# Kernel optimization log

Hardware: AMD Instinct MI355X
Metric: run time of the kernel (lower is better)

The kernel has to match this reference:

```python
import jax, jax.numpy as jnp
import numpy as np
from jax import lax

N = 1024          # proposals per image
C = 81            # classes incl. background
F = 1024          # feature dim
K = 100           # detections_per_img
IMG_W, IMG_H = 1216.0, 800.0
SCORE_THRESH = 0.05
NMS_THRESH = 0.5
BBOX_CLIP = float(np.log(1000.0 / 16.0))
WX, WY, WW, WH = 10.0, 10.0, 5.0, 5.0     # BoxCoder default weights


def setup_inputs() -> dict:
    key = jax.random.key(0)
    k1, k2, k3, k4, k5 = jax.random.split(key, 5)
    class_logits = jax.random.normal(k1, (N, C), jnp.float32) * 2.0
    box_regression = jax.random.normal(k2, (N, C * 4), jnp.float32) * 0.2
    xy = jax.random.uniform(k3, (N, 2), jnp.float32) * jnp.array([IMG_W * 0.7, IMG_H * 0.7], jnp.float32)
    wh = 16.0 + jax.random.uniform(k4, (N, 2), jnp.float32) * jnp.array([IMG_W * 0.3, IMG_H * 0.3], jnp.float32)
    proposal_boxes = jnp.concatenate([xy, xy + wh], axis=1)  # valid xyxy
    features = jax.random.normal(k5, (N, F), jnp.float32)
    return {"class_logits": class_logits, "box_regression": box_regression,
            "proposal_boxes": proposal_boxes, "features": features}


def _decode(rel, boxes):
    # BoxCoder.decode with weights (10,10,5,5), TO_REMOVE=1. rel:[N,C*4] boxes:[N,4] -> [N,C,4]
    rel = rel.reshape(N, C, 4)
    widths = boxes[:, 2] - boxes[:, 0] + 1.0
    heights = boxes[:, 3] - boxes[:, 1] + 1.0
    ctr_x = boxes[:, 0] + 0.5 * widths
    ctr_y = boxes[:, 1] + 0.5 * heights
    dx = rel[..., 0] / WX
    dy = rel[..., 1] / WY
    dw = jnp.minimum(rel[..., 2] / WW, BBOX_CLIP)
    dh = jnp.minimum(rel[..., 3] / WH, BBOX_CLIP)
    pcx = dx * widths[:, None] + ctr_x[:, None]
    pcy = dy * heights[:, None] + ctr_y[:, None]
    pw = jnp.exp(dw) * widths[:, None]
    ph = jnp.exp(dh) * heights[:, None]
    return jnp.stack([pcx - 0.5 * pw, pcy - 0.5 * ph,
                      pcx + 0.5 * pw - 1.0, pcy + 0.5 * ph - 1.0], axis=-1)


def _clip(b):
    # clip_to_image with TO_REMOVE=1
    x1 = jnp.clip(b[..., 0], 0.0, IMG_W - 1.0)
    y1 = jnp.clip(b[..., 1], 0.0, IMG_H - 1.0)
    x2 = jnp.clip(b[..., 2], 0.0, IMG_W - 1.0)
    y2 = jnp.clip(b[..., 3], 0.0, IMG_H - 1.0)
    return jnp.stack([x1, y1, x2, y2], axis=-1)


def _nms_class(boxes_c, scores_c, valid_c):
    # Sequential hard NMS for one class with fixed shapes. Invalid (below score
    # thresh) boxes can neither be kept nor suppress others.
    s_sort = jnp.where(valid_c, scores_c, -jnp.inf)
    order = jnp.argsort(-s_sort)              # descending score
    b = boxes_c[order]
    v = valid_c[order]
    s = scores_c[order]
    area = (b[:, 2] - b[:, 0] + 1.0) * (b[:, 3] - b[:, 1] + 1.0)
    lt = jnp.maximum(b[:, None, :2], b[None, :, :2])
    rb = jnp.minimum(b[:, None, 2:], b[None, :, 2:])
    whd = jnp.clip(rb - lt + 1.0, 0.0)
    inter = whd[..., 0] * whd[..., 1]
    iou = inter / (area[:, None] + area[None, :] - inter)  # [N,N]
    idx = jnp.arange(N)
    def body(i, keep):
        sup = (iou[i] > NMS_THRESH) & keep[i] & (idx > i)
        return keep & ~sup
    keep = lax.fori_loop(0, N, body, v)
    return b, order, jnp.where(keep, s, -1.0)


def reference(class_logits, box_regression, proposal_boxes, features):
    probs = jax.nn.softmax(class_logits, axis=-1)          # [N,C]
    dec = _clip(_decode(box_regression, proposal_boxes))    # [N,C,4]
    boxes_cls = jnp.transpose(dec[:, 1:, :], (1, 0, 2))     # [C-1,N,4] (skip background)
    scores_cls = probs[:, 1:].T                             # [C-1,N]
    valid = scores_cls > SCORE_THRESH
    b_s, order, s_kept = jax.vmap(_nms_class)(boxes_cls, scores_cls, valid)
    flat_s = s_kept.reshape(-1)                             # [(C-1)*N]
    top_s, top_i = lax.top_k(flat_s, K)
    cls_i = top_i // N
    pos_i = top_i % N
    boxes_out = b_s[cls_i, pos_i]                           # [K,4]
    orig = order[cls_i, pos_i]                              # original proposal idx
    feat_out = features[orig]                               # [K,F]
    labels = cls_i + 1
    ok = top_s > 0.0
    scores_out = jnp.where(ok, top_s, 0.0)
    boxes_out = jnp.where(ok[:, None], boxes_out, 0.0)
    feat_out = jnp.where(ok[:, None], feat_out, 0.0)
    labels = jnp.where(ok, labels, 0)
    return boxes_out, scores_out, feat_out, labels
```

## Files before the change

kernel.cpp:

```cpp
#include <hip/hip_runtime.h>
#include <math.h>

#define N 1024
#define C 81
#define F 1024
#define K 100
#define NC1 80
#define MAXC (NC1 * N)
#define HBASE 0x3D00
#define HSIZE 1024
#define SELCAP 2048

#define SCORE_THRESH 0.05f
#define NMS_THRESH   0.5f
#define BBOX_CLIP    4.135166556742356f
#define IMG_W1       1215.0f
#define IMG_H1       799.0f

typedef unsigned long long u64;
typedef unsigned int u32;

__global__ __launch_bounds__(256) void k_softmax_decode(
    const float* __restrict__ logits, const float* __restrict__ boxreg,
    const float* __restrict__ pboxes, float* __restrict__ probsT,
    float4* __restrict__ decT, int* __restrict__ hist, int* __restrict__ counter)
{
    int gid = blockIdx.x * 256 + threadIdx.x;
    if (gid < HSIZE) hist[gid] = 0;
    if (gid == 0) *counter = 0;

    int n = blockIdx.x * 4 + (threadIdx.x >> 6);
    int t = threadIdx.x & 63;

    float v1 = logits[n * C + t];
    float v2 = (t < C - 64) ? logits[n * C + 64 + t] : -INFINITY;
    float m = fmaxf(v1, v2);
    for (int off = 32; off; off >>= 1) m = fmaxf(m, __shfl_xor(m, off));
    float e1 = expf(v1 - m);
    float e2 = (t < C - 64) ? expf(v2 - m) : 0.0f;
    float s = e1 + e2;
    for (int off = 32; off; off >>= 1) s += __shfl_xor(s, off);

    probsT[t * N + n] = e1 / s;
    if (t < C - 64) probsT[(64 + t) * N + n] = e2 / s;

    float bx1 = pboxes[n * 4 + 0], by1 = pboxes[n * 4 + 1];
    float bx2 = pboxes[n * 4 + 2], by2 = pboxes[n * 4 + 3];
    float w  = bx2 - bx1 + 1.0f, h = by2 - by1 + 1.0f;
    float cx = bx1 + 0.5f * w,  cy = by1 + 0.5f * h;

    #pragma unroll
    for (int rep = 0; rep < 2; ++rep) {
        int cl = t + rep * 64;
        if (cl >= C) break;
        const float* r = boxreg + (size_t)n * (C * 4) + cl * 4;
        float dx = r[0] / 10.0f, dy = r[1] / 10.0f;
        float dw = fminf(r[2] / 5.0f, BBOX_CLIP);
        float dh = fminf(r[3] / 5.0f, BBOX_CLIP);

        float pcx = dx * w + cx, pcy = dy * h + cy;
        float pw = expf(dw) * w, ph = expf(dh) * h;

        float x1 = pcx - 0.5f * pw,        y1 = pcy - 0.5f * ph;
        float x2 = pcx + 0.5f * pw - 1.0f, y2 = pcy + 0.5f * ph - 1.0f;

        x1 = fminf(fmaxf(x1, 0.0f), IMG_W1);
        y1 = fminf(fmaxf(y1, 0.0f), IMG_H1);
        x2 = fminf(fmaxf(x2, 0.0f), IMG_W1);
        y2 = fminf(fmaxf(y2, 0.0f), IMG_H1);

        decT[(size_t)cl * N + n] = make_float4(x1, y1, x2, y2);
    }
}

__global__ __launch_bounds__(256) void k_nms(
    const float* __restrict__ probsT, const float4* __restrict__ decT,
    int* counter, u64* __restrict__ ckey, int* __restrict__ hist,
    int* __restrict__ corder)
{
    int c = blockIdx.x;
    int t = threadIdx.x;
    __shared__ u64    skey64[N];
    __shared__ int    scnt[256];
    __shared__ float4 sbox[N];
    __shared__ float  sarea[N];
    __shared__ int    skeep[N];

    const float4* prow = (const float4*)(probsT + (size_t)(c + 1) * N);
    float4 s4 = prow[t];
    int f0 = s4.x > SCORE_THRESH, f1 = s4.y > SCORE_THRESH;
    int f2 = s4.z > SCORE_THRESH, f3 = s4.w > SCORE_THRESH;
    int mycount = f0 + f1 + f2 + f3;
    scnt[t] = mycount;
    __syncthreads();
    for (int off = 1; off < 256; off <<= 1) {
        int v = scnt[t];
        int a = (t >= off) ? scnt[t - off] : 0;
        __syncthreads();
        scnt[t] = v + a;
        __syncthreads();
    }
    int base = scnt[t] - mycount;
    int V = scnt[255];
    {
        int p0 = t * 4, pos = base;
        if (f0) skey64[pos++] = ((u64)__float_as_uint(s4.x) << 32) | (u32)~(u32)(p0);
        if (f1) skey64[pos++] = ((u64)__float_as_uint(s4.y) << 32) | (u32)~(u32)(p0 + 1);
        if (f2) skey64[pos++] = ((u64)__float_as_uint(s4.z) << 32) | (u32)~(u32)(p0 + 2);
        if (f3) skey64[pos++] = ((u64)__float_as_uint(s4.w) << 32) | (u32)~(u32)(p0 + 3);
    }
    __syncthreads();
    if (V == 0) return;

    if (V <= 64) {
        if (t < 64) {
            int lane = t;
            u64 key = (lane < V) ? skey64[lane] : 0ull;
            for (int k = 2; k <= 64; k <<= 1) {
                for (int j = k >> 1; j > 0; j >>= 1) {
                    u64 other = __shfl_xor(key, j);
                    bool takeMax = (((lane & j) == 0) == ((lane & k) == 0));
                    bool gt = key > other;
                    key = (takeMax == gt) ? key : other;
                }
            }
            bool act = key != 0ull;
            float4 b = make_float4(0.f, 0.f, 0.f, 0.f);
            float area = 0.0f;
            if (act) {
                int idx = (int)(~(u32)(key & 0xffffffffu));
                corder[c * N + lane] = idx;
                b = decT[(size_t)(c + 1) * N + idx];
                area = (b.z - b.x + 1.0f) * (b.w - b.y + 1.0f);
            }
            int kept = act ? 1 : 0;
            for (int i = 0; i + 1 < V; ++i) {
                int   ki  = __shfl(kept, i);
                float bix = __shfl(b.x, i), biy = __shfl(b.y, i);
                float biz = __shfl(b.z, i), biw = __shfl(b.w, i);
                float ai  = __shfl(area, i);
                if (ki && lane > i && kept) {
                    float lx = fmaxf(bix, b.x), ly = fmaxf(biy, b.y);
                    float rx = fminf(biz, b.z), ry = fminf(biw, b.w);
                    float ww = fmaxf(rx - lx + 1.0f, 0.0f);
                    float hh = fmaxf(ry - ly + 1.0f, 0.0f);
                    float inter = ww * hh;
                    float iou = inter / (ai + area - inter);
                    if (iou > NMS_THRESH) kept = 0;
                }
            }
            if (kept) {
                int pos = atomicAdd(counter, 1);
                u32 sb = (u32)(key >> 32);
                ckey[pos] = ((u64)sb << 32) | (u64)(u32)~(u32)(c * N + lane);
                atomicAdd(&hist[(int)(sb >> 16) - HBASE], 1);
            }
        }
        return;
    }

    int P = 128;
    while (P < V) P <<= 1;
    for (int i = V + t; i < P; i += 256) skey64[i] = 0ull;
    __syncthreads();
    for (int k = 2; k <= P; k <<= 1) {
        for (int j = k >> 1; j > 0; j >>= 1) {
            for (int i = t; i < P; i += 256) {
                int ixj = i ^ j;
                if (ixj > i) {
                    u64 a = skey64[i], bb = skey64[ixj];
                    bool desc = ((i & k) == 0);
                    if (desc ? (a < bb) : (a > bb)) { skey64[i] = bb; skey64[ixj] = a; }
                }
            }
            __syncthreads();
        }
    }
    for (int p = t; p < V; p += 256) {
        int idx = (int)(~(u32)(skey64[p] & 0xffffffffu));
        corder[c * N + p] = idx;
        float4 b = decT[(size_t)(c + 1) * N + idx];
        sbox[p]  = b;
        sarea[p] = (b.z - b.x + 1.0f) * (b.w - b.y + 1.0f);
        skeep[p] = 1;
    }
    __syncthreads();
    for (int i = 0; i < V; ++i) {
        if (skeep[i]) {
            float4 bi = sbox[i];
            float  ai = sarea[i];
            for (int j = i + 1 + t; j < V; j += 256) {
                if (skeep[j]) {
                    float4 bj = sbox[j];
                    float lx = fmaxf(bi.x, bj.x), ly = fmaxf(bi.y, bj.y);
                    float rx = fminf(bi.z, bj.z), ry = fminf(bi.w, bj.w);
                    float ww = fmaxf(rx - lx + 1.0f, 0.0f);
                    float hh = fmaxf(ry - ly + 1.0f, 0.0f);
                    float inter = ww * hh;
                    float iou = inter / (ai + sarea[j] - inter);
                    if (iou > NMS_THRESH) skeep[j] = 0;
                }
            }
        }
        __syncthreads();
    }
    for (int p = t; p < V; p += 256) {
        if (skeep[p]) {
            int pos = atomicAdd(counter, 1);
            u32 sb = (u32)(skey64[p] >> 32);
            ckey[pos] = ((u64)sb << 32) | (u64)(u32)~(u32)(c * N + p);
            atomicAdd(&hist[(int)(sb >> 16) - HBASE], 1);
        }
    }
}

__global__ __launch_bounds__(1024) void k_select(
    const int* __restrict__ counter, u64* ckey, const int* __restrict__ hist,
    float* __restrict__ sel_score, int* __restrict__ sel_flat)
{
    int t = threadIdx.x;
    __shared__ u64 keys[SELCAP];
    __shared__ int partial[1024];
    __shared__ int sb_bstar, scount;
    __shared__ u64 wk[16];
    __shared__ int wp[16];

    int M = *counter;
    if (t == 0) { sb_bstar = 0; scount = 0; }

    int lsum = hist[t];
    partial[t] = lsum;
    __syncthreads();
    for (int off = 1; off < 1024; off <<= 1) {
        int v = partial[t];
        int a = (t + off < 1024) ? partial[t + off] : 0;
        __syncthreads();
        partial[t] = v + a;
        __syncthreads();
    }
    int base = partial[t] - lsum;
    if (base < K && base + lsum >= K) sb_bstar = t;
    __syncthreads();
    int bstar = sb_bstar;

    for (int p = t; p < M; p += 1024) {
        u64 kk = ckey[p];
        int b = (int)((kk >> 48) & 0xFFFF) - HBASE;
        if (b >= bstar) {
            int pos = atomicAdd(&scount, 1);
            if (pos < SELCAP) keys[pos] = kk;
        }
    }
    __syncthreads();
    int cnt = scount;

    if (cnt > SELCAP) {
        for (int k = 0; k < K; ++k) {
            u64 key = 0ull; int pos = -1;
            for (int p = t; p < M; p += 1024) {
                u64 kk = ckey[p];
                if (kk > key) { key = kk; pos = p; }
            }
            for (int off = 32; off; off >>= 1) {
                u64 ok2 = __shfl_down(key, off);
                int op = __shfl_down(pos, off);
                if (ok2 > key) { key = ok2; pos = op; }
            }
            if ((t & 63) == 0) { wk[t >> 6] = key; wp[t >> 6] = pos; }
            __syncthreads();
            if (t == 0) {
                for (int w = 1; w < 16; ++w)
                    if (wk[w] > key) { key = wk[w]; pos = wp[w]; }
                if (key != 0ull) {
                    sel_score[k] = __uint_as_float((u32)(key >> 32));
                    sel_flat[k]  = (int)(~(u32)(key & 0xffffffffu));
                    ckey[pos] = 0ull;
                } else { sel_score[k] = 0.0f; sel_flat[k] = 0; }
            }
            __syncthreads();
        }
        return;
    }

    int P = 128;
    while (P < cnt) P <<= 1;
    for (int i = cnt + t; i < P; i += 1024) keys[i] = 0ull;
    __syncthreads();
    for (int k = 2; k <= P; k <<= 1) {
        for (int j = k >> 1; j > 0; j >>= 1) {
            for (int i = t; i < P; i += 1024) {
                int ixj = i ^ j;
                if (ixj > i) {
                    u64 a = keys[i], b = keys[ixj];
                    bool desc = ((i & k) == 0);
                    if (desc ? (a < b) : (a > b)) { keys[i] = b; keys[ixj] = a; }
                }
            }
            __syncthreads();
        }
    }
    if (t < K) {
        u64 key = keys[t];
        sel_score[t] = __uint_as_float((u32)(key >> 32));
        sel_flat[t]  = (int)(~(u32)(key & 0xffffffffu));
    }
}

__global__ __launch_bounds__(256) void k_gather(
    const float* __restrict__ sel_score, const int* __restrict__ sel_flat,
    const int* __restrict__ corder, const float4* __restrict__ decT,
    const float* __restrict__ feats, float* __restrict__ out)
{
    int k = blockIdx.x, t = threadIdx.x;
    float s = sel_score[k];
    bool ok = s > 0.0f;
    float4 b = make_float4(0.f, 0.f, 0.f, 0.f);
    int label = 0, orig = 0;
    if (ok) {
        int flat = sel_flat[k];
        int c = flat >> 10;
        orig  = corder[flat];
        b     = decT[(size_t)(c + 1) * N + orig];
        label = c + 1;
    }
    if (t == 0) {
        out[k * 4 + 0] = b.x; out[k * 4 + 1] = b.y;
        out[k * 4 + 2] = b.z; out[k * 4 + 3] = b.w;
        out[K * 4 + k] = ok ? s : 0.0f;
        out[K * 4 + K + K * F + k] = (float)label;
    }
    const float4* src = (const float4*)(feats + (size_t)orig * F);
    float4* dst = (float4*)(out + K * 4 + K + (size_t)k * F);
    float4 z = make_float4(0.f, 0.f, 0.f, 0.f);
    if (t < F / 4) dst[t] = ok ? src[t] : z;
}

extern "C" void kernel_launch(void* const* d_in, const int* in_sizes, int n_in,
                              void* d_out, int out_size, void* d_ws, size_t ws_size,
                              hipStream_t stream)
{
    const float* logits = (const float*)d_in[0];
    const float* boxreg = (const float*)d_in[1];
    const float* pboxes = (const float*)d_in[2];
    const float* feats  = (const float*)d_in[3];
    float* out = (float*)d_out;

    char* ws = (char*)d_ws;
    size_t off = 0;
    auto alloc = [&](size_t bytes) {
        size_t cur = off;
        off = (off + bytes + 255) & ~(size_t)255;
        return cur;
    };
    int*    counter   = (int*)   (ws + alloc(sizeof(int)));
    float*  probsT    = (float*) (ws + alloc(sizeof(float)  * C * N));
    float4* decT      = (float4*)(ws + alloc(sizeof(float4) * C * N));
    u64*    ckey      = (u64*)   (ws + alloc(sizeof(u64)    * MAXC));
    int*    hist      = (int*)   (ws + alloc(sizeof(int)    * HSIZE));
    int*    corder    = (int*)   (ws + alloc(sizeof(int)    * NC1 * N));
    float*  sel_score = (float*) (ws + alloc(sizeof(float)  * K));
    int*    sel_flat  = (int*)   (ws + alloc(sizeof(int)    * K));

    hipLaunchKernelGGL(k_softmax_decode, dim3(N / 4), dim3(256), 0, stream,
                       logits, boxreg, pboxes, probsT, decT, hist, counter);
    hipLaunchKernelGGL(k_nms, dim3(NC1), dim3(256), 0, stream,
                       probsT, decT, counter, ckey, hist, corder);
    hipLaunchKernelGGL(k_select, dim3(1), dim3(1024), 0, stream,
                       counter, ckey, hist, sel_score, sel_flat);
    hipLaunchKernelGGL(k_gather, dim3(K), dim3(256), 0, stream,
                       sel_score, sel_flat, corder, decT, feats, out);
}
```

Baseline: 107.7 us.

## Fuse softmax and box decode into per-class NMS kernel, drop intermediate buffers

```diff
diff --git a/kernel.cpp b/kernel.cpp
--- a/kernel.cpp
+++ b/kernel.cpp
@@ -20,76 +20,75 @@
 typedef unsigned long long u64;
 typedef unsigned int u32;
 
-__global__ __launch_bounds__(256) void k_softmax_decode(
+__device__ float4 decode_box(const float* __restrict__ pboxes,
+                             const float* __restrict__ boxreg, int idx, int cl)
+{
+    float4 pb = ((const float4*)pboxes)[idx];
+    float4 r  = *(const float4*)(boxreg + (size_t)idx * (C * 4) + cl * 4);
+    float w  = pb.z - pb.x + 1.0f, h = pb.w - pb.y + 1.0f;
+    float cx = pb.x + 0.5f * w,  cy = pb.y + 0.5f * h;
+    float dx = r.x / 10.0f, dy = r.y / 10.0f;
+    float dw = fminf(r.z / 5.0f, BBOX_CLIP);
+    float dh = fminf(r.w / 5.0f, BBOX_CLIP);
+    float pcx = dx * w + cx, pcy = dy * h + cy;
+    float pw = expf(dw) * w, ph = expf(dh) * h;
+    float x1 = pcx - 0.5f * pw,        y1 = pcy - 0.5f * ph;
+    float x2 = pcx + 0.5f * pw - 1.0f, y2 = pcy + 0.5f * ph - 1.0f;
+    x1 = fminf(fmaxf(x1, 0.0f), IMG_W1);
+    y1 = fminf(fmaxf(y1, 0.0f), IMG_H1);
+    x2 = fminf(fmaxf(x2, 0.0f), IMG_W1);
+    y2 = fminf(fmaxf(y2, 0.0f), IMG_H1);
+    return make_float4(x1, y1, x2, y2);
+}
+
+__global__ __launch_bounds__(1024) void k_init(int* __restrict__ hist,
+                                               int* __restrict__ counter)
+{
+    int t = threadIdx.x;
+    hist[t] = 0;
+    if (t == 0) *counter = 0;
+}
+
+__global__ __launch_bounds__(256) void k_class(
     const float* __restrict__ logits, const float* __restrict__ boxreg,
-    const float* __restrict__ pboxes, float* __restrict__ probsT,
-    float4* __restrict__ decT, int* __restrict__ hist, int* __restrict__ counter)
-{
-    int gid = blockIdx.x * 256 + threadIdx.x;
-    if (gid < HSIZE) hist[gid] = 0;
-    if (gid == 0) *counter = 0;
-
-    int n = blockIdx.x * 4 + (threadIdx.x >> 6);
-    int t = threadIdx.x & 63;
-
-    float v1 = logits[n * C + t];
-    float v2 = (t < C - 64) ? logits[n * C + 64 + t] : -INFINITY;
-    float m = fmaxf(v1, v2);
-    for (int off = 32; off; off >>= 1) m = fmaxf(m, __shfl_xor(m, off));
-    float e1 = expf(v1 - m);
-    float e2 = (t < C - 64) ? expf(v2 - m) : 0.0f;
-    float s = e1 + e2;
-    for (int off = 32; off; off >>= 1) s += __shfl_xor(s, off);
-
-    probsT[t * N + n] = e1 / s;
-    if (t < C - 64) probsT[(64 + t) * N + n] = e2 / s;
-
-    float bx1 = pboxes[n * 4 + 0], by1 = pboxes[n * 4 + 1];
-    float bx2 = pboxes[n * 4 + 2], by2 = pboxes[n * 4 + 3];
-    float w  = bx2 - bx1 + 1.0f, h = by2 - by1 + 1.0f;
-    float cx = bx1 + 0.5f * w,  cy = by1 + 0.5f * h;
-
-    #pragma unroll
-    for (int rep = 0; rep < 2; ++rep) {
-        int cl = t + rep * 64;
-        if (cl >= C) break;
-        const float* r = boxreg + (size_t)n * (C * 4) + cl * 4;
-        float dx = r[0] / 10.0f, dy = r[1] / 10.0f;
-        float dw = fminf(r[2] / 5.0f, BBOX_CLIP);
-        float dh = fminf(r[3] / 5.0f, BBOX_CLIP);
-
-        float pcx = dx * w + cx, pcy = dy * h + cy;
-        float pw = expf(dw) * w, ph = expf(dh) * h;
-
-        float x1 = pcx - 0.5f * pw,        y1 = pcy - 0.5f * ph;
-        float x2 = pcx + 0.5f * pw - 1.0f, y2 = pcy + 0.5f * ph - 1.0f;
-
-        x1 = fminf(fmaxf(x1, 0.0f), IMG_W1);
-        y1 = fminf(fmaxf(y1, 0.0f), IMG_H1);
-        x2 = fminf(fmaxf(x2, 0.0f), IMG_W1);
-        y2 = fminf(fmaxf(y2, 0.0f), IMG_H1);
-
-        decT[(size_t)cl * N + n] = make_float4(x1, y1, x2, y2);
-    }
-}
-
-__global__ __launch_bounds__(256) void k_nms(
-    const float* __restrict__ probsT, const float4* __restrict__ decT,
-    int* counter, u64* __restrict__ ckey, int* __restrict__ hist,
-    int* __restrict__ corder)
+    const float* __restrict__ pboxes, u64* __restrict__ ckey,
+    float4* __restrict__ cbox, int* __restrict__ corig,
+    int* __restrict__ hist, int* __restrict__ counter)
 {
     int c = blockIdx.x;
     int t = threadIdx.x;
+    int wave = t >> 6, lane64 = t & 63;
+    __shared__ float  sscore[N];
     __shared__ u64    skey64[N];
     __shared__ int    scnt[256];
     __shared__ float4 sbox[N];
     __shared__ float  sarea[N];
     __shared__ int    skeep[N];
 
-    const float4* prow = (const float4*)(probsT + (size_t)(c + 1) * N);
-    float4 s4 = prow[t];
-    int f0 = s4.x > SCORE_THRESH, f1 = s4.y > SCORE_THRESH;
-    int f2 = s4.z > SCORE_THRESH, f3 = s4.w > SCORE_THRESH;
+    {
+        int cl = c + 1;
+        #pragma unroll 4
+        for (int r = wave; r < N; r += 4) {
+            float v1 = logits[r * C + lane64];
+            float v2 = (lane64 < C - 64) ? logits[r * C + 64 + lane64] : -INFINITY;
+            float m = fmaxf(v1, v2);
+            for (int off = 32; off; off >>= 1) m = fmaxf(m, __shfl_xor(m, off));
+            float e1 = expf(v1 - m);
+            float e2 = (lane64 < C - 64) ? expf(v2 - m) : 0.0f;
+            float s = e1 + e2;
+            for (int off = 32; off; off >>= 1) s += __shfl_xor(s, off);
+            float ec = (cl < 64) ? __shfl(e1, cl) : __shfl(e2, cl - 64);
+            if (lane64 == 0) sscore[r] = ec / s;
+        }
+    }
+    __syncthreads();
+
+    float s0 = sscore[t];
+    float s1 = sscore[t + 256];
+    float s2 = sscore[t + 512];
+    float s3 = sscore[t + 768];
+    int f0 = s0 > SCORE_THRESH, f1 = s1 > SCORE_THRESH;
+    int f2 = s2 > SCORE_THRESH, f3 = s3 > SCORE_THRESH;
     int mycount = f0 + f1 + f2 + f3;
     scnt[t] = mycount;
     __syncthreads();
@@ -103,11 +102,11 @@
     int base = scnt[t] - mycount;
     int V = scnt[255];
     {
-        int p0 = t * 4, pos = base;
-        if (f0) skey64[pos++] = ((u64)__float_as_uint(s4.x) << 32) | (u32)~(u32)(p0);
-        if (f1) skey64[pos++] = ((u64)__float_as_uint(s4.y) << 32) | (u32)~(u32)(p0 + 1);
-        if (f2) skey64[pos++] = ((u64)__float_as_uint(s4.z) << 32) | (u32)~(u32)(p0 + 2);
-        if (f3) skey64[pos++] = ((u64)__float_as_uint(s4.w) << 32) | (u32)~(u32)(p0 + 3);
+        int pos = base;
+        if (f0) skey64[pos++] = ((u64)__float_as_uint(s0) << 32) | (u32)~(u32)(t);
+        if (f1) skey64[pos++] = ((u64)__float_as_uint(s1) << 32) | (u32)~(u32)(t + 256);
+        if (f2) skey64[pos++] = ((u64)__float_as_uint(s2) << 32) | (u32)~(u32)(t + 512);
+        if (f3) skey64[pos++] = ((u64)__float_as_uint(s3) << 32) | (u32)~(u32)(t + 768);
     }
     __syncthreads();
     if (V == 0) return;
@@ -129,9 +128,10 @@
             float area = 0.0f;
             if (act) {
                 int idx = (int)(~(u32)(key & 0xffffffffu));
-                corder[c * N + lane] = idx;
-                b = decT[(size_t)(c + 1) * N + idx];
+                b = decode_box(pboxes, boxreg, idx, c + 1);
                 area = (b.z - b.x + 1.0f) * (b.w - b.y + 1.0f);
+                cbox[c * N + lane]  = b;
+                corig[c * N + lane] = idx;
             }
             int kept = act ? 1 : 0;
             for (int i = 0; i + 1 < V; ++i) {
@@ -178,11 +178,12 @@
     }
     for (int p = t; p < V; p += 256) {
         int idx = (int)(~(u32)(skey64[p] & 0xffffffffu));
-        corder[c * N + p] = idx;
-        float4 b = decT[(size_t)(c + 1) * N + idx];
+        float4 b = decode_box(pboxes, boxreg, idx, c + 1);
         sbox[p]  = b;
         sarea[p] = (b.z - b.x + 1.0f) * (b.w - b.y + 1.0f);
         skeep[p] = 1;
+        cbox[c * N + p]  = b;
+        corig[c * N + p] = idx;
     }
     __syncthreads();
     for (int i = 0; i < V; ++i) {
@@ -308,7 +309,7 @@
 
 __global__ __launch_bounds__(256) void k_gather(
     const float* __restrict__ sel_score, const int* __restrict__ sel_flat,
-    const int* __restrict__ corder, const float4* __restrict__ decT,
+    const int* __restrict__ corig, const float4* __restrict__ cbox,
     const float* __restrict__ feats, float* __restrict__ out)
 {
     int k = blockIdx.x, t = threadIdx.x;
@@ -318,10 +319,9 @@
     int label = 0, orig = 0;
     if (ok) {
         int flat = sel_flat[k];
-        int c = flat >> 10;
-        orig  = corder[flat];
-        b     = decT[(size_t)(c + 1) * N + orig];
-        label = c + 1;
+        orig  = corig[flat];
+        b     = cbox[flat];
+        label = (flat >> 10) + 1;
     }
     if (t == 0) {
         out[k * 4 + 0] = b.x; out[k * 4 + 1] = b.y;
@@ -352,21 +352,19 @@
         off = (off + bytes + 255) & ~(size_t)255;
         return cur;
     };
+    u64*    ckey      = (u64*)   (ws + alloc(sizeof(u64)    * MAXC));
+    float4* cbox      = (float4*)(ws + alloc(sizeof(float4) * NC1 * N));
+    int*    corig     = (int*)   (ws + alloc(sizeof(int)    * NC1 * N));
+    int*    hist      = (int*)   (ws + alloc(sizeof(int)    * HSIZE));
     int*    counter   = (int*)   (ws + alloc(sizeof(int)));
-    float*  probsT    = (float*) (ws + alloc(sizeof(float)  * C * N));
-    float4* decT      = (float4*)(ws + alloc(sizeof(float4) * C * N));
-    u64*    ckey      = (u64*)   (ws + alloc(sizeof(u64)    * MAXC));
-    int*    hist      = (int*)   (ws + alloc(sizeof(int)    * HSIZE));
-    int*    corder    = (int*)   (ws + alloc(sizeof(int)    * NC1 * N));
     float*  sel_score = (float*) (ws + alloc(sizeof(float)  * K));
     int*    sel_flat  = (int*)   (ws + alloc(sizeof(int)    * K));
 
-    hipLaunchKernelGGL(k_softmax_decode, dim3(N / 4), dim3(256), 0, stream,
-                       logits, boxreg, pboxes, probsT, decT, hist, counter);
-    hipLaunchKernelGGL(k_nms, dim3(NC1), dim3(256), 0, stream,
-                       probsT, decT, counter, ckey, hist, corder);
+    hipLaunchKernelGGL(k_init, dim3(1), dim3(1024), 0, stream, hist, counter);
+    hipLaunchKernelGGL(k_class, dim3(NC1), dim3(256), 0, stream,
+                       logits, boxreg, pboxes, ckey, cbox, corig, hist, counter);
     hipLaunchKernelGGL(k_select, dim3(1), dim3(1024), 0, stream,
                        counter, ckey, hist, sel_score, sel_flat);
     hipLaunchKernelGGL(k_gather, dim3(K), dim3(256), 0, stream,
-                       sel_score, sel_flat, corder, decT, feats, out);
-}
+                       sel_score, sel_flat, corig, cbox, feats, out);
+}
```

After: 298.6 us. 2.77x slower.
